# Optimization experiments

Measured on AMD Instinct MI355X. Metric: run time of the kernel, lower is better.

The kernel has to match this reference:

```python
import jax, jax.numpy as jnp
import numpy as np

N_NODES, N_EDGES, HID = 30000, 480000, 128
N_GRAPHS, N_CLASSES = 128, 6
BN_EPS, ADD_SCORE = 1e-5, 0.5


def setup_inputs():
    key = jax.random.key(0)
    ks = jax.random.split(key, 12)
    g = lambda i, shape: jax.random.normal(ks[i], shape, jnp.float32) * 0.05
    return dict(
        x=jax.random.normal(ks[0], (N_NODES, HID), jnp.float32),
        edge_index=jax.random.randint(ks[1], (2, N_EDGES), 0, N_NODES, jnp.int32),
        batch=jnp.sort(jax.random.randint(ks[2], (N_NODES,), 0, N_GRAPHS, jnp.int32)),
        Wl=g(3, (6, HID, HID)), bl=jnp.zeros((6, HID), jnp.float32),
        Wr=g(4, (6, HID, HID)),
        gamma=jnp.ones((6, HID), jnp.float32), beta=jnp.zeros((6, HID), jnp.float32),
        Wlin=g(5, (3, HID, 2 * HID)), blin=jnp.zeros((3, HID), jnp.float32),
        Wp=g(6, (3, 2 * HID)), bp=jnp.zeros((3,), jnp.float32),
        Wf1=g(7, (HID, HID)), bf1=jnp.zeros((HID,), jnp.float32),
        Wf2=g(8, (N_CLASSES, HID)), bf2=jnp.zeros((N_CLASSES,), jnp.float32),
    )


def _sage(x, src, dst, emf, Wl_i, bl_i, Wr_i, N):
    # PyG SAGEConv: lin_l(mean_{j->i} x_j) + lin_r(x_i); emf masks dead edges
    msg = x[src] * emf[:, None]                              # [E,H]
    s = jax.ops.segment_sum(msg, dst, num_segments=N)
    c = jax.ops.segment_sum(emf, dst, num_segments=N)
    mean = s / jnp.maximum(c, 1.0)[:, None]
    return mean @ Wl_i.T + bl_i + x @ Wr_i.T


def _bn(x, g, b, nvf):
    # training-mode BatchNorm over valid (non-merged-away) nodes only
    cnt = jnp.maximum(nvf.sum(), 1.0)
    mu = (x * nvf[:, None]).sum(0) / cnt
    var = (((x - mu) ** 2) * nvf[:, None]).sum(0) / cnt
    return g * (x - mu) * jax.lax.rsqrt(var + BN_EPS) + b


def _edge_pool(x, src, dst, emb, nvb, Wp_i, bp_i, N, E):
    h = x.shape[1]
    # raw edge score = Linear(cat(x[src], x[dst]))
    raw = (x @ Wp_i[:h])[src] + (x @ Wp_i[h:])[dst] + bp_i   # [E]
    neg = jnp.finfo(x.dtype).min
    mx = jax.ops.segment_max(jnp.where(emb, raw, neg), dst, num_segments=N)
    z = jnp.where(emb, jnp.exp(jnp.where(emb, raw - mx[dst], 0.0)), 0.0)
    den = jax.ops.segment_sum(z, dst, num_segments=N)
    score = z / jnp.maximum(den, 1e-16)[dst] + ADD_SCORE     # softmax per dst + 0.5

    # greedy edge matching in descending score order (sequential, int-only carry)
    order = jnp.argsort(-jnp.where(emb, jax.lax.stop_gradient(score), -jnp.inf))

    def step(carry, i):
        matched, cluster, chosen = carry
        s, t = src[i], dst[i]
        ok = emb[i] & (~matched[s]) & (~matched[t]) & (s != t)
        rep, oth = jnp.minimum(s, t), jnp.maximum(s, t)
        matched = matched.at[s].set(matched[s] | ok)
        matched = matched.at[t].set(matched[t] | ok)
        cluster = cluster.at[oth].set(jnp.where(ok, rep, cluster[oth]))
        chosen = chosen.at[rep].set(jnp.where(ok, i, chosen[rep]))
        return (matched, cluster, chosen), None

    init = (~nvb, jnp.arange(N, dtype=jnp.int32), jnp.full((N,), -1, jnp.int32))
    (matched, cluster, chosen), _ = jax.lax.scan(step, init, order)

    # merged node = (x_s + x_t) * score(chosen edge); singleton score = 1
    nscore = jnp.where(chosen >= 0, score[jnp.maximum(chosen, 0)], 1.0)
    new_x = jax.ops.segment_sum(x, cluster, num_segments=N) * nscore[:, None]
    nvb2 = nvb & (cluster == jnp.arange(N, dtype=jnp.int32))
    # remap edges to cluster representatives; coalesce duplicates (self-loops kept, as PyG)
    key = jnp.where(emb, cluster[src] * N + cluster[dst], -1)  # N*N < 2**31
    uk = jnp.unique(key, size=E, fill_value=-1)
    emb2 = uk >= 0
    ukc = jnp.maximum(uk, 0)
    return new_x, ukc // N, ukc % N, emb2, nvb2


def reference(x, edge_index, batch, Wl, bl, Wr, gamma, beta, Wlin, blin, Wp, bp, Wf1, bf1, Wf2, bf2):
    N, E = x.shape[0], edge_index.shape[1]
    src, dst = edge_index[0], edge_index[1]
    emb = jnp.ones((E,), bool)   # edge-valid mask (fixed-shape graph coarsening)
    nvb = jnp.ones((N,), bool)   # node-valid mask
    for blk in range(3):
        emf, nvf = emb.astype(x.dtype), nvb.astype(x.dtype)
        i = 2 * blk
        h = _bn(jax.nn.relu(_sage(x, src, dst, emf, Wl[i], bl[i], Wr[i], N)), gamma[i], beta[i], nvf)
        h2 = _bn(jax.nn.relu(_sage(h, src, dst, emf, Wl[i + 1], bl[i + 1], Wr[i + 1], N)), gamma[i + 1], beta[i + 1], nvf)
        x = jnp.concatenate([h2, h], axis=1) @ Wlin[blk].T + blin[blk]  # dropout = identity (eval)
        x, src, dst, emb, nvb = _edge_pool(x, src, dst, emb, nvb, Wp[blk], bp[blk], N, E)
    nvf = nvb.astype(x.dtype)
    sums = jax.ops.segment_sum(x * nvf[:, None], batch, num_segments=N_GRAPHS)
    cnt = jax.ops.segment_sum(nvf, batch, num_segments=N_GRAPHS)
    pooled = sums / jnp.maximum(cnt, 1.0)[:, None]           # global_mean_pool
    hfc = jax.nn.relu(pooled @ Wf1.T + bf1)
    return jax.nn.log_softmax(hfc @ Wf2.T + bf2, axis=1)
```

## Files before the change

### kernel.cpp

```cpp
#include <hip/hip_runtime.h>
#include <stdint.h>

#define NN 30000
#define NE 480000
#define HID 128
#define NG 128
#define NC 6
#define BN_EPS 1e-5f
#define WPB 938
#define SLOTS 4
#define GPAD 132

typedef unsigned int u32;
typedef unsigned long long u64;

__device__ __forceinline__ u64 ent_key(int4 ent) {
  return ((u64)(u32)ent.y << 32) | (u32)ent.x;
}

__global__ void k_init(const int* __restrict__ ei, int* srcA, int* dstA, int* nvb,
                       int* scal, int* b3, int* i2, float* gbuf) {
  int t = blockIdx.x * 256 + threadIdx.x;
  if (t < NE) { srcA[t] = ei[t]; dstA[t] = ei[NE + t]; }
  if (t < NN) nvb[t] = 1;
  if (t < 2 * NN) { b3[t] = 0; i2[t] = 0; }
  if (t < NG * HID + NG) gbuf[t] = 0.f;
  if (t == 0) { scal[0] = NE; scal[1] = 0; }
}

__global__ void k_csr_count(const int* __restrict__ pE, const int* __restrict__ src,
                            const int* __restrict__ dst, int* __restrict__ cnt,
                            int* __restrict__ icnt, const int* __restrict__ nvb,
                            int* __restrict__ pcnt) {
  int t = blockIdx.x * 256 + threadIdx.x;
  if (t < NN && nvb[t]) atomicAdd(pcnt, 1);
  if (t < *pE) {
    int s = src[t], d = dst[t];
    atomicAdd(&cnt[d], 1);
    if (s != d) { atomicAdd(&icnt[s], 1); atomicAdd(&icnt[d], 1); }
  }
}

__global__ __launch_bounds__(1024) void k_scan2(const int* __restrict__ in0, int* __restrict__ out0,
                                                const int* __restrict__ in1, int* __restrict__ out1) {
  const int* in = blockIdx.x ? in1 : in0;
  int* out = blockIdx.x ? out1 : out0;
  __shared__ int part[1024];
  int t = threadIdx.x;
  int chunk = (NN + 1023) / 1024;
  int b = t * chunk, e = b + chunk;
  if (b > NN) b = NN;
  if (e > NN) e = NN;
  int s = 0;
  for (int i = b; i < e; i++) s += in[i];
  part[t] = s;
  __syncthreads();
  for (int off = 1; off < 1024; off <<= 1) {
    int v = (t >= off) ? part[t - off] : 0;
    __syncthreads();
    part[t] += v;
    __syncthreads();
  }
  int excl = (t == 0) ? 0 : part[t - 1];
  for (int i = b; i < e; i++) { out[i] = excl; excl += in[i]; }
  if (t == 0) out[NN] = part[1023];
}

__global__ void k_csr_scatter(const int* __restrict__ pE, const int* __restrict__ src,
                              const int* __restrict__ dst, const int* __restrict__ coff,
                              int* __restrict__ cursor, int* __restrict__ eids,
                              int* __restrict__ gsrc) {
  int e = blockIdx.x * 256 + threadIdx.x;
  if (e >= *pE) return;
  int d = dst[e];
  int pos = coff[d] + atomicAdd(&cursor[d], 1);
  eids[pos] = e;
  gsrc[pos] = src[e];
}

__global__ __launch_bounds__(256) void k_sage_gather(
    const int* __restrict__ coff, const int* __restrict__ gsrc,
    const float* __restrict__ x, float* __restrict__ mean,
    double* __restrict__ bnsum) {
  if (blockIdx.x == 0 && threadIdx.x < 2 * HID) bnsum[threadIdx.x] = 0.0;
  int grp = threadIdx.x >> 5;
  int lane = threadIdx.x & 31;
  int n = blockIdx.x * 8 + grp;
  if (n >= NN) return;
  int b = coff[n], e2 = coff[n + 1];
  float4 acc = make_float4(0.f, 0.f, 0.f, 0.f);
  int i = b;
  for (; i + 1 < e2; i += 2) {
    int s0 = gsrc[i], s1 = gsrc[i + 1];
    float4 v0 = *(const float4*)(x + (size_t)s0 * HID + lane * 4);
    float4 v1 = *(const float4*)(x + (size_t)s1 * HID + lane * 4);
    acc.x += v0.x; acc.y += v0.y; acc.z += v0.z; acc.w += v0.w;
    acc.x += v1.x; acc.y += v1.y; acc.z += v1.z; acc.w += v1.w;
  }
  if (i < e2) {
    int s0 = gsrc[i];
    float4 v0 = *(const float4*)(x + (size_t)s0 * HID + lane * 4);
    acc.x += v0.x; acc.y += v0.y; acc.z += v0.z; acc.w += v0.w;
  }
  float inv = 1.0f / fmaxf((float)(e2 - b), 1.0f);
  acc.x *= inv; acc.y *= inv; acc.z *= inv; acc.w *= inv;
  *(float4*)(mean + (size_t)n * HID + lane * 4) = acc;
}

__global__ __launch_bounds__(256) void gemm_dual2(
    const float* __restrict__ A1, const float* __restrict__ W1,
    const float* __restrict__ A2, const float* __restrict__ W2,
    const float* __restrict__ bias, float* __restrict__ out,
    int M, int ldw, int relu, const int* __restrict__ nvb,
    double* __restrict__ bnsum, int dostats) {
  __shared__ float Ast[16][GPAD];
  __shared__ float Ws[16][GPAD];
  int tid = threadIdx.x;
  int rg = tid >> 4, cg = tid & 15;
  int r0 = rg * 8, c0 = cg * 8;
  int row0 = blockIdx.x * 128;
  float acc[8][8];
#pragma unroll
  for (int a = 0; a < 8; a++)
#pragma unroll
    for (int bq = 0; bq < 8; bq++) acc[a][bq] = 0.f;

  for (int srcI = 0; srcI < 2; srcI++) {
    const float* A = srcI ? A2 : A1;
    const float* W = srcI ? W2 : W1;
    for (int kc = 0; kc < 128; kc += 16) {
#pragma unroll
      for (int i = 0; i < 2; i++) {
        int k = tid + i * 256;
        int r = k >> 2, c4 = (k & 3) << 2;
        int gr = row0 + r;
        float4 v = make_float4(0.f, 0.f, 0.f, 0.f);
        if (gr < M) v = *(const float4*)(A + (size_t)gr * 128 + kc + c4);
        Ast[c4 + 0][r] = v.x; Ast[c4 + 1][r] = v.y;
        Ast[c4 + 2][r] = v.z; Ast[c4 + 3][r] = v.w;
        float4 w = *(const float4*)(W + (size_t)r * ldw + kc + c4);
        Ws[c4 + 0][r] = w.x; Ws[c4 + 1][r] = w.y;
        Ws[c4 + 2][r] = w.z; Ws[c4 + 3][r] = w.w;
      }
      __syncthreads();
#pragma unroll
      for (int kk = 0; kk < 16; kk++) {
        float4 a0 = *(const float4*)(&Ast[kk][r0]);
        float4 a1 = *(const float4*)(&Ast[kk][r0 + 4]);
        float4 b0 = *(const float4*)(&Ws[kk][c0]);
        float4 b1 = *(const float4*)(&Ws[kk][c0 + 4]);
        float av[8] = {a0.x, a0.y, a0.z, a0.w, a1.x, a1.y, a1.z, a1.w};
        float bv[8] = {b0.x, b0.y, b0.z, b0.w, b1.x, b1.y, b1.z, b1.w};
#pragma unroll
        for (int rr = 0; rr < 8; rr++)
#pragma unroll
          for (int cc = 0; cc < 8; cc++) acc[rr][cc] += av[rr] * bv[cc];
      }
      __syncthreads();
    }
  }

  float sCol[8], qCol[8];
#pragma unroll
  for (int cc = 0; cc < 8; cc++) { sCol[cc] = 0.f; qCol[cc] = 0.f; }
#pragma unroll
  for (int rr = 0; rr < 8; rr++) {
    int gr = row0 + r0 + rr;
    if (gr >= M) continue;
    int valid = dostats ? nvb[gr] : 0;
    float vv[8];
#pragma unroll
    for (int cc = 0; cc < 8; cc++) {
      float v = acc[rr][cc] + bias[c0 + cc];
      if (relu) v = fmaxf(v, 0.f);
      vv[cc] = v;
      if (valid) { sCol[cc] += v; qCol[cc] += v * v; }
    }
    *(float4*)(out + (size_t)gr * 128 + c0) = make_float4(vv[0], vv[1], vv[2], vv[3]);
    *(float4*)(out + (size_t)gr * 128 + c0 + 4) = make_float4(vv[4], vv[5], vv[6], vv[7]);
  }
  if (dostats) {
#pragma unroll
    for (int cc = 0; cc < 8; cc++) { Ast[rg][c0 + cc] = sCol[cc]; Ws[rg][c0 + cc] = qCol[cc]; }
    __syncthreads();
    if (tid < HID) {
      float s = 0.f, q = 0.f;
#pragma unroll
      for (int g = 0; g < 16; g++) { s += Ast[g][tid]; q += Ws[g][tid]; }
      atomicAdd(&bnsum[tid], (double)s);
      atomicAdd(&bnsum[HID + tid], (double)q);
    }
  }
}

__global__ void k_bn_apply(float* __restrict__ x, const double* __restrict__ sums,
                           const int* __restrict__ cnt, const float* __restrict__ gamma,
                           const float* __restrict__ beta) {
  int t = blockIdx.x * 256 + threadIdx.x;
  if (t >= NN * HID) return;
  int k = t & 127;
  double c = (double)((*cnt > 1) ? *cnt : 1);
  double mu = sums[k] / c;
  double var = sums[HID + k] / c - mu * mu;
  if (var < 0.0) var = 0.0;
  float inv = (float)(1.0 / sqrt(var + (double)BN_EPS));
  x[t] = gamma[k] * (x[t] - (float)mu) * inv + beta[k];
}

__global__ void k_node_proj(const float* __restrict__ x, const float* __restrict__ Wp,
                            float* __restrict__ px1, float* __restrict__ px2) {
  int n = blockIdx.x * 256 + threadIdx.x;
  if (n >= NN) return;
  const float* xr = x + (size_t)n * HID;
  float s1 = 0.f, s2 = 0.f;
#pragma unroll 8
  for (int k = 0; k < HID; k += 4) {
    float4 v = *(const float4*)(xr + k);
    float4 w1 = *(const float4*)(Wp + k);
    float4 w2 = *(const float4*)(Wp + HID + k);
    s1 += v.x * w1.x + v.y * w1.y + v.z * w1.z + v.w * w1.w;
    s2 += v.x * w2.x + v.y * w2.y + v.z * w2.z + v.w * w2.w;
  }
  px1[n] = s1; px2[n] = s2;
}

__global__ void k_edge_softmax_seed(
    const int* __restrict__ coff, const int* __restrict__ eids,
    const int* __restrict__ gsrc, const float* __restrict__ px1,
    const float* __restrict__ px2, const float* __restrict__ bp,
    float* __restrict__ score, u64* __restrict__ ekey, u64* __restrict__ S) {
  int n = blockIdx.x * 256 + threadIdx.x;
  if (n >= NN) return;
  S[n] = 0ull;
  int b = coff[n], e2 = coff[n + 1];
  if (b == e2) return;
  float p2 = px2[n] + *bp;
  float mx = -3.4e38f;
  for (int i = b; i < e2; i++) {
    float r = px1[gsrc[i]] + p2;
    mx = fmaxf(mx, r);
  }
  double den = 0.0;
  for (int i = b; i < e2; i++) {
    int eid = eids[i];
    float z = expf(px1[gsrc[i]] + p2 - mx);
    score[eid] = z;
    den += (double)z;
  }
  if (den < 1e-16) den = 1e-16;
  double invd = 1.0 / den;
  for (int i = b; i < e2; i++) {
    int eid = eids[i];
    float sc = (float)((double)score[eid] * invd) + 0.5f;
    score[eid] = sc;
    ekey[eid] = ((u64)__float_as_uint(sc) << 32) | (u64)(0xFFFFFFFFu - (u32)eid);
  }
}

__global__ void k_inc_scatter(const int* __restrict__ pE, const int* __restrict__ src,
                              const int* __restrict__ dst, const u64* __restrict__ ekey,
                              const int* __restrict__ ioff, int* __restrict__ icur,
                              int4* __restrict__ ielist) {
  int e = blockIdx.x * 256 + threadIdx.x;
  if (e >= *pE) return;
  int s = src[e], d = dst[e];
  if (s == d) return;
  u64 k = ekey[e];
  int4 ent;
  ent.x = (int)(u32)(k & 0xFFFFFFFFull);
  ent.y = (int)(u32)(k >> 32);
  ent.w = 0;
  ent.z = d;
  ielist[ioff[s] + atomicAdd(&icur[s], 1)] = ent;
  ent.z = s;
  ielist[ioff[d] + atomicAdd(&icur[d], 1)] = ent;
}

__global__ __launch_bounds__(256) void k_suitor(
    const int* __restrict__ ioff, const int4* __restrict__ ielist,
    const int* __restrict__ src, const int* __restrict__ dst,
    u64* __restrict__ S) {
  int wid = threadIdx.x >> 6;
  int lane = threadIdx.x & 63;
  int n = blockIdx.x * 4 + wid;
  if (n >= NN) return;
  int cur = n;
  while (cur >= 0) {
    int b = ioff[cur], e2 = ioff[cur + 1];
    int deg = e2 - b;
    if (deg == 0) break;
    if (deg <= 64 * SLOTS) {
      u64 key[SLOTS]; int pv[SLOTS];
#pragma unroll
      for (int s = 0; s < SLOTS; s++) {
        key[s] = 0; pv[s] = 0;
        int i = b + s * 64 + lane;
        if (i < e2) {
          int4 ent = ielist[i];
          key[s] = ent_key(ent);
          pv[s] = ent.z;
        }
      }
      long long res;
      for (;;) {
        u64 localBest = 0;
#pragma unroll
        for (int s = 0; s < SLOTS; s++) {
          if (!key[s]) continue;
          u64 sv = __hip_atomic_load(&S[pv[s]], __ATOMIC_RELAXED, __HIP_MEMORY_SCOPE_AGENT);
          if (sv >= key[s]) key[s] = 0;
          else if (key[s] > localBest) localBest = key[s];
        }
        u64 bestKey = localBest;
#pragma unroll
        for (int o = 32; o > 0; o >>= 1) {
          u64 other = __shfl_xor(bestKey, o, 64);
          if (other > bestKey) bestKey = other;
        }
        if (bestKey == 0) { res = -1; break; }
        int ms = -1;
#pragma unroll
        for (int s = 0; s < SLOTS; s++)
          if (ms < 0 && key[s] == bestKey) ms = s;
        u64 ball = __ballot(ms >= 0);
        int owner = (int)(__ffsll((long long)ball) - 1);
        long long r0 = -3;
        if (lane == owner) {
          int bv = pv[ms];
          u64 old = atomicMax(&S[bv], bestKey);
          if (old >= bestKey) { key[ms] = 0; r0 = -2; }
          else if (old == 0) r0 = -1;
          else {
            int eo = (int)(0xFFFFFFFFu - (u32)(old & 0xFFFFFFFFull));
            int so = src[eo], do_ = dst[eo];
            r0 = (so == bv) ? do_ : so;
          }
        }
        res = __shfl(r0, owner, 64);
        if (res != -2) break;
      }
      if (res < 0) break;
      cur = (int)res;
    } else {
      u64 bestKey = 0;
      for (int i = b + lane; i < e2; i += 64) {
        int4 ent = ielist[i];
        u64 k = ent_key(ent);
        if (k <= bestKey) continue;
        u64 sv = __hip_atomic_load(&S[ent.z], __ATOMIC_RELAXED, __HIP_MEMORY_SCOPE_AGENT);
        if (k > sv) bestKey = k;
      }
#pragma unroll
      for (int o = 32; o > 0; o >>= 1) {
        u64 other = __shfl_xor(bestKey, o, 64);
        if (other > bestKey) bestKey = other;
      }
      long long r0 = -1;
      if (bestKey != 0 && lane == 0) {
        int e = (int)(0xFFFFFFFFu - (u32)(bestKey & 0xFFFFFFFFull));
        int es = src[e], ed = dst[e];
        int bv = (es == cur) ? ed : es;
        u64 old = atomicMax(&S[bv], bestKey);
        if (old >= bestKey) r0 = cur;
        else if (old != 0) {
          int eo = (int)(0xFFFFFFFFu - (u32)(old & 0xFFFFFFFFull));
          int so = src[eo], do_ = dst[eo];
          r0 = (so == bv) ? do_ : so;
        }
      }
      long long res = (bestKey != 0) ? __shfl(r0, 0, 64) : -1;
      cur = (int)res;
    }
  }
}

__global__ __launch_bounds__(256) void k_new_x(
    const u64* __restrict__ S, const int* __restrict__ src, const int* __restrict__ dst,
    const float* __restrict__ score, const float* __restrict__ x,
    float* __restrict__ out, int* __restrict__ cluster,
    int* __restrict__ nvb, int* __restrict__ b3zero) {
  int gt = blockIdx.x * 256 + threadIdx.x;
  if (gt < 2 * NN) b3zero[gt] = 0;
  int grp = threadIdx.x >> 5;
  int lane = threadIdx.x & 31;
  int n = blockIdx.x * 8 + grp;
  if (n >= NN) return;
  u64 k = S[n];
  int partner = -1;
  int rep = n;
  bool isOth = false;
  float sc = 1.f;
  if (k) {
    int e = (int)(0xFFFFFFFFu - (u32)(k & 0xFFFFFFFFull));
    int s = src[e], d = dst[e];
    int other = (s == n) ? d : s;
    if (S[other] == k) {
      if (n > other) { isOth = true; rep = other; }
      else { partner = other; sc = score[e]; }
    }
  }
  float4 v = make_float4(0.f, 0.f, 0.f, 0.f);
  if (!isOth) {
    v = *(const float4*)(x + (size_t)n * HID + lane * 4);
    if (partner >= 0) {
      float4 w = *(const float4*)(x + (size_t)partner * HID + lane * 4);
      v.x = (v.x + w.x) * sc; v.y = (v.y + w.y) * sc;
      v.z = (v.z + w.z) * sc; v.w = (v.w + w.w) * sc;
    }
  }
  *(float4*)(out + (size_t)n * HID + lane * 4) = v;
  if (lane == 0) {
    cluster[n] = rep;
    nvb[n] = (nvb[n] && !isOth) ? 1 : 0;
  }
}

__global__ void k_bucket_count(const int* __restrict__ pE, const int* __restrict__ src,
                               const int* __restrict__ cluster, int* __restrict__ bcount) {
  int e = blockIdx.x * 256 + threadIdx.x;
  if (e >= *pE) return;
  atomicAdd(&bcount[cluster[src[e]]], 1);
}

__global__ __launch_bounds__(1024) void k_scan(const int* __restrict__ in, int* __restrict__ out,
                                               int n, int* totalDst) {
  __shared__ int part[1024];
  int t = threadIdx.x;
  int chunk = (n + 1023) / 1024;
  int b = t * chunk, e = b + chunk;
  if (b > n) b = n;
  if (e > n) e = n;
  int s = 0;
  for (int i = b; i < e; i++) s += in[i];
  part[t] = s;
  __syncthreads();
  for (int off = 1; off < 1024; off <<= 1) {
    int v = (t >= off) ? part[t - off] : 0;
    __syncthreads();
    part[t] += v;
    __syncthreads();
  }
  int excl = (t == 0) ? 0 : part[t - 1];
  int total = part[1023];
  for (int i = b; i < e; i++) { out[i] = excl; excl += in[i]; }
  if (t == 0) {
    out[n] = total;
    if (totalDst) *totalDst = total;
  }
}

__global__ void k_bucket_scatter(const int* __restrict__ pE, const int* __restrict__ src,
                                 const int* __restrict__ dst, const int* __restrict__ cluster,
                                 const int* __restrict__ boffs, int* __restrict__ bcursor,
                                 int* __restrict__ bucket) {
  int e = blockIdx.x * 256 + threadIdx.x;
  if (e >= *pE) return;
  int cs = cluster[src[e]], cd = cluster[dst[e]];
  int pos = boffs[cs] + atomicAdd(&bcursor[cs], 1);
  bucket[pos] = cd;
}

__global__ __launch_bounds__(256) void k_dedup_bitmap(
    const int* __restrict__ boffs, int* __restrict__ bucket,
    int* __restrict__ ucount) {
  __shared__ u32 bm[4][960];
  int wid = threadIdx.x >> 6;
  int lane = threadIdx.x & 63;
  int n = blockIdx.x * 4 + wid;
  int b = boffs[n], e = boffs[n + 1];
  for (int w = lane; w < 960; w += 64) bm[wid][w] = 0;
  __syncthreads();
  for (int i = b + lane; i < e; i += 64)
    atomicOr(&bm[wid][bucket[i] >> 5], 1u << (bucket[i] & 31));
  __syncthreads();
  int w0 = lane * 15;
  int w1 = w0 + 15; if (w1 > WPB) w1 = WPB;
  int cnt = 0;
  for (int w = w0; w < w1; w++) cnt += __popc(bm[wid][w]);
  int inc = cnt;
  for (int o = 1; o < 64; o <<= 1) { int v = __shfl_up(inc, o); if (lane >= o) inc += v; }
  int excl = inc - cnt;
  int total = __shfl(inc, 63);
  int pos = b + excl;
  for (int w = w0; w < w1; w++) {
    u32 v = bm[wid][w];
    while (v) { int bit = __ffs(v) - 1; bucket[pos++] = (w << 5) | bit; v &= v - 1; }
  }
  if (lane == 0) ucount[n] = total;
}

__global__ void k_emit(const int* __restrict__ boffs, const int* __restrict__ bucket,
                       const int* __restrict__ bucount, const int* __restrict__ bnoffs,
                       int* __restrict__ srcO, int* __restrict__ dstO,
                       int* __restrict__ b3zero, int* __restrict__ i2zero,
                       int* __restrict__ pcnt) {
  int t = blockIdx.x * 256 + threadIdx.x;
  int stride = gridDim.x * 256;
  for (int z = t; z < 2 * NN; z += stride) { b3zero[z] = 0; i2zero[z] = 0; }
  if (t == 0) *pcnt = 0;
  if (t >= NN) return;
  int u = bucount[t], b = boffs[t], o = bnoffs[t];
  for (int i = 0; i < u; i++) { srcO[o + i] = t; dstO[o + i] = bucket[b + i]; }
}

__global__ void k_graph_pool(const int* __restrict__ nvb, const int* __restrict__ batch,
                             const float* __restrict__ x, float* __restrict__ gsum,
                             float* __restrict__ gcnt) {
  int t = blockIdx.x * 256 + threadIdx.x;
  int n = t >> 2;
  if (n >= NN) return;
  if (!nvb[n]) return;
  int sub = t & 3;
  int g = batch[n];
  const float* xr = x + (size_t)n * HID + sub * 32;
  float* o = gsum + (size_t)g * HID + sub * 32;
#pragma unroll
  for (int i = 0; i < 8; i++) {
    float4 v = *(const float4*)(xr + i * 4);
    atomicAdd(o + i * 4 + 0, v.x); atomicAdd(o + i * 4 + 1, v.y);
    atomicAdd(o + i * 4 + 2, v.z); atomicAdd(o + i * 4 + 3, v.w);
  }
  if (sub == 0) atomicAdd(&gcnt[g], 1.0f);
}

__global__ __launch_bounds__(128) void k_head1(const float* __restrict__ gsum,
                                               const float* __restrict__ gcnt,
                                               const float* __restrict__ Wf1,
                                               const float* __restrict__ bf1,
                                               float* __restrict__ hfc) {
  int g = blockIdx.x;
  int j = threadIdx.x;
  __shared__ float p[HID];
  float c = fmaxf(gcnt[g], 1.f);
  p[j] = gsum[g * HID + j] / c;
  __syncthreads();
  float s = bf1[j];
  const float* w = Wf1 + (size_t)j * HID;
  for (int k = 0; k < HID; k++) s += p[k] * w[k];
  hfc[g * HID + j] = fmaxf(s, 0.f);
}

__global__ void k_head2(const float* __restrict__ hfc, const float* __restrict__ Wf2,
                        const float* __restrict__ bf2, float* __restrict__ out) {
  int g = blockIdx.x;
  int t = threadIdx.x;
  __shared__ float lg[NC];
  if (t < NC) {
    float s = bf2[t];
    const float* w = Wf2 + (size_t)t * HID;
    const float* h = hfc + (size_t)g * HID;
    for (int k = 0; k < HID; k++) s += h[k] * w[k];
    lg[t] = s;
  }
  __syncthreads();
  if (t == 0) {
    float m = lg[0];
    for (int c = 1; c < NC; c++) m = fmaxf(m, lg[c]);
    float se = 0.f;
    for (int c = 0; c < NC; c++) se += expf(lg[c] - m);
    float lse = m + logf(se);
    for (int c = 0; c < NC; c++) out[g * NC + c] = lg[c] - lse;
  }
}

extern "C" void kernel_launch(void* const* d_in, const int* in_sizes, int n_in,
                              void* d_out, int out_size, void* d_ws, size_t ws_size,
                              hipStream_t stream) {
  const float* x0 = (const float*)d_in[0];
  const int* ei = (const int*)d_in[1];
  const int* batch = (const int*)d_in[2];
  const float* Wl = (const float*)d_in[3];
  const float* bl = (const float*)d_in[4];
  const float* Wr = (const float*)d_in[5];
  const float* gamma = (const float*)d_in[6];
  const float* beta = (const float*)d_in[7];
  const float* Wlin = (const float*)d_in[8];
  const float* blin = (const float*)d_in[9];
  const float* Wp = (const float*)d_in[10];
  const float* bp = (const float*)d_in[11];
  const float* Wf1 = (const float*)d_in[12];
  const float* bf1 = (const float*)d_in[13];
  const float* Wf2 = (const float*)d_in[14];
  const float* bf2 = (const float*)d_in[15];
  float* out = (float*)d_out;

  const int NH = NN * HID;
  size_t off = 0;
  char* base = (char*)d_ws;
  auto carve = [&](size_t bytes) -> char* {
    char* p = base + off;
    off += (bytes + 255) & ~(size_t)255;
    return p;
  };
  float* xa = (float*)carve((size_t)NH * 4);
  float* xb = (float*)carve((size_t)NH * 4);
  float* xc = (float*)carve((size_t)NH * 4);
  float* xd = (float*)carve((size_t)NH * 4);
  int* srcA = (int*)carve((size_t)NE * 4);
  int* dstA = (int*)carve((size_t)NE * 4);
  int* srcB = (int*)carve((size_t)NE * 4);
  int* dstB = (int*)carve((size_t)NE * 4);
  float* escore = (float*)carve((size_t)NE * 4);
  int* ebucket = (int*)carve((size_t)NE * 4);
  int* eids = (int*)carve((size_t)NE * 4);
  int* gsrc = (int*)carve((size_t)NE * 4);
  u64* ekey = (u64*)carve((size_t)NE * 8);
  u64* S = (u64*)carve((size_t)NN * 8);
  float* npx1 = (float*)carve((size_t)NN * 4);
  float* npx2 = (float*)carve((size_t)NN * 4);
  int* ncluster = (int*)carve((size_t)NN * 4);
  int* nvb = (int*)carve((size_t)NN * 4);
  int* b3 = (int*)carve((size_t)3 * NN * 4);
  int* bcount = b3;
  int* bcursor = b3 + NN;
  int* bucount = b3 + 2 * NN;
  int* i2 = (int*)carve((size_t)2 * NN * 4);
  int* icnt = i2;
  int* icursor = i2 + NN;
  int* boffs = (int*)carve((size_t)(NN + 1) * 4);
  int* bnoffs = (int*)carve((size_t)(NN + 1) * 4);
  int* csroff = (int*)carve((size_t)(NN + 1) * 4);
  int* ioff = (int*)carve((size_t)(NN + 1) * 4);
  double* bnsum = (double*)carve((size_t)2 * HID * 8);
  float* gbuf = (float*)carve((size_t)(NG * HID + NG) * 4);
  float* gsum = gbuf;
  float* gcnt = gbuf + NG * HID;
  float* ghfc = (float*)carve((size_t)NG * HID * 4);
  int* scal = (int*)carve(64 * 4);
  (void)ws_size; (void)n_in; (void)in_sizes; (void)out_size;

  int4* ielist = (int4*)xc;

  int* pE = scal;
  int* pcnt = scal + 1;

  k_init<<<1875, 256, 0, stream>>>(ei, srcA, dstA, nvb, scal, b3, i2, gbuf);

  int* srcC = srcA; int* dstC = dstA; int* srcN = srcB; int* dstN = dstB;
  float* xcur = xa;
  float* xtmp = xd;

  auto sage = [&](const float* xin, float* xout, int L) {
    k_sage_gather<<<3750, 256, 0, stream>>>(csroff, gsrc, xin, xtmp, bnsum);
    gemm_dual2<<<235, 256, 0, stream>>>(xtmp, Wl + (size_t)L * HID * HID, xin,
                                        Wr + (size_t)L * HID * HID, bl + (size_t)L * HID,
                                        xout, NN, HID, 1, nvb, bnsum, 1);
    k_bn_apply<<<15000, 256, 0, stream>>>(xout, bnsum, pcnt, gamma + (size_t)L * HID,
                                          beta + (size_t)L * HID);
  };

  for (int b = 0; b < 3; b++) {
    const float* xin = (b == 0) ? x0 : (const float*)xcur;

    k_csr_count<<<1875, 256, 0, stream>>>(pE, srcC, dstC, bcount, icnt, nvb, pcnt);
    k_scan2<<<2, 1024, 0, stream>>>(bcount, csroff, icnt, ioff);
    k_csr_scatter<<<1875, 256, 0, stream>>>(pE, srcC, dstC, csroff, bcursor, eids, gsrc);

    sage(xin, xb, 2 * b);
    sage(xb, xc, 2 * b + 1);
    gemm_dual2<<<235, 256, 0, stream>>>(xc, Wlin + (size_t)b * HID * 2 * HID, xb,
                                        Wlin + (size_t)b * HID * 2 * HID + HID,
                                        blin + (size_t)b * HID, xcur, NN, 2 * HID, 0,
                                        nvb, bnsum, 0);

    k_node_proj<<<118, 256, 0, stream>>>(xcur, Wp + (size_t)b * 2 * HID, npx1, npx2);
    k_edge_softmax_seed<<<118, 256, 0, stream>>>(csroff, eids, gsrc, npx1, npx2, bp + b,
                                                 escore, ekey, S);
    k_inc_scatter<<<1875, 256, 0, stream>>>(pE, srcC, dstC, ekey, ioff, icursor, ielist);
    k_suitor<<<7500, 256, 0, stream>>>(ioff, ielist, srcC, dstC, S);
    k_new_x<<<3750, 256, 0, stream>>>(S, srcC, dstC, escore, xcur, xtmp,
                                      ncluster, nvb, b3);

    if (b < 2) {
      k_bucket_count<<<1875, 256, 0, stream>>>(pE, srcC, ncluster, bcount);
      k_scan<<<1, 1024, 0, stream>>>(bcount, boffs, NN, (int*)nullptr);
      k_bucket_scatter<<<1875, 256, 0, stream>>>(pE, srcC, dstC, ncluster, boffs, bcursor,
                                                 ebucket);
      k_dedup_bitmap<<<7500, 256, 0, stream>>>(boffs, ebucket, bucount);
      k_scan<<<1, 1024, 0, stream>>>(bucount, bnoffs, NN, pE);
      k_emit<<<235, 256, 0, stream>>>(boffs, ebucket, bucount, bnoffs, srcN, dstN,
                                      b3, i2, pcnt);
      { int* t = srcC; srcC = srcN; srcN = t; t = dstC; dstC = dstN; dstN = t; }
    }
    { float* t = xcur; xcur = xtmp; xtmp = t; }
  }

  k_graph_pool<<<469, 256, 0, stream>>>(nvb, batch, xcur, gsum, gcnt);
  k_head1<<<NG, 128, 0, stream>>>(gsum, gcnt, Wf1, bf1, ghfc);
  k_head2<<<NG, 32, 0, stream>>>(ghfc, Wf2, bf2, out);
}
```

Baseline: 2.544 ms.

## Fold BatchNorm into next GEMM load, fuse node projection, restructure suitor kernel

```diff
diff --git a/kernel.cpp b/kernel.cpp
--- a/kernel.cpp
+++ b/kernel.cpp
@@ -19,12 +19,14 @@
 }
 
 __global__ void k_init(const int* __restrict__ ei, int* srcA, int* dstA, int* nvb,
-                       int* scal, int* b3, int* i2, float* gbuf) {
+                       int* scal, int* b3, int* i2, float* gbuf,
+                       double* __restrict__ bnsum) {
   int t = blockIdx.x * 256 + threadIdx.x;
   if (t < NE) { srcA[t] = ei[t]; dstA[t] = ei[NE + t]; }
   if (t < NN) nvb[t] = 1;
   if (t < 2 * NN) { b3[t] = 0; i2[t] = 0; }
   if (t < NG * HID + NG) gbuf[t] = 0.f;
+  if (t < 2 * HID) bnsum[t] = 0.0;
   if (t == 0) { scal[0] = NE; scal[1] = 0; }
 }
 
@@ -80,9 +82,7 @@
 
 __global__ __launch_bounds__(256) void k_sage_gather(
     const int* __restrict__ coff, const int* __restrict__ gsrc,
-    const float* __restrict__ x, float* __restrict__ mean,
-    double* __restrict__ bnsum) {
-  if (blockIdx.x == 0 && threadIdx.x < 2 * HID) bnsum[threadIdx.x] = 0.0;
+    const float* __restrict__ x, float* __restrict__ mean) {
   int grp = threadIdx.x >> 5;
   int lane = threadIdx.x & 31;
   int n = blockIdx.x * 8 + grp;
@@ -112,7 +112,10 @@
     const float* __restrict__ A2, const float* __restrict__ W2,
     const float* __restrict__ bias, float* __restrict__ out,
     int M, int ldw, int relu, const int* __restrict__ nvb,
-    double* __restrict__ bnsum, int dostats) {
+    double* __restrict__ bnsum, int dostats,
+    const float* __restrict__ a1f, const float* __restrict__ c1f,
+    const float* __restrict__ a2f, const float* __restrict__ c2f,
+    const float* __restrict__ Wp, float* __restrict__ px1, float* __restrict__ px2) {
   __shared__ float Ast[16][GPAD];
   __shared__ float Ws[16][GPAD];
   int tid = threadIdx.x;
@@ -128,6 +131,8 @@
   for (int srcI = 0; srcI < 2; srcI++) {
     const float* A = srcI ? A2 : A1;
     const float* W = srcI ? W2 : W1;
+    const float* fa = srcI ? a2f : a1f;
+    const float* fc = srcI ? c2f : c1f;
     for (int kc = 0; kc < 128; kc += 16) {
 #pragma unroll
       for (int i = 0; i < 2; i++) {
@@ -136,6 +141,12 @@
         int gr = row0 + r;
         float4 v = make_float4(0.f, 0.f, 0.f, 0.f);
         if (gr < M) v = *(const float4*)(A + (size_t)gr * 128 + kc + c4);
+        if (fa) {
+          float4 av = *(const float4*)(fa + kc + c4);
+          float4 cv = *(const float4*)(fc + kc + c4);
+          v.x = v.x * av.x + cv.x; v.y = v.y * av.y + cv.y;
+          v.z = v.z * av.z + cv.z; v.w = v.w * av.w + cv.w;
+        }
         Ast[c4 + 0][r] = v.x; Ast[c4 + 1][r] = v.y;
         Ast[c4 + 2][r] = v.z; Ast[c4 + 3][r] = v.w;
         float4 w = *(const float4*)(W + (size_t)r * ldw + kc + c4);
@@ -160,24 +171,45 @@
     }
   }
 
+  float wp1[8], wp2[8];
+  if (Wp) {
+#pragma unroll
+    for (int cc = 0; cc < 8; cc++) { wp1[cc] = Wp[c0 + cc]; wp2[cc] = Wp[HID + c0 + cc]; }
+  }
+  float* part1 = (float*)Ast;
+  float* part2 = (float*)Ws;
   float sCol[8], qCol[8];
 #pragma unroll
   for (int cc = 0; cc < 8; cc++) { sCol[cc] = 0.f; qCol[cc] = 0.f; }
 #pragma unroll
   for (int rr = 0; rr < 8; rr++) {
     int gr = row0 + r0 + rr;
-    if (gr >= M) continue;
-    int valid = dostats ? nvb[gr] : 0;
-    float vv[8];
-#pragma unroll
-    for (int cc = 0; cc < 8; cc++) {
-      float v = acc[rr][cc] + bias[c0 + cc];
-      if (relu) v = fmaxf(v, 0.f);
-      vv[cc] = v;
-      if (valid) { sCol[cc] += v; qCol[cc] += v * v; }
+    float p1 = 0.f, p2 = 0.f;
+    if (gr < M) {
+      int valid = dostats ? nvb[gr] : 0;
+      float vv[8];
+#pragma unroll
+      for (int cc = 0; cc < 8; cc++) {
+        float v = acc[rr][cc] + bias[c0 + cc];
+        if (relu) v = fmaxf(v, 0.f);
+        vv[cc] = v;
+        if (valid) { sCol[cc] += v; qCol[cc] += v * v; }
+        if (Wp) { p1 += v * wp1[cc]; p2 += v * wp2[cc]; }
+      }
+      *(float4*)(out + (size_t)gr * 128 + c0) = make_float4(vv[0], vv[1], vv[2], vv[3]);
+      *(float4*)(out + (size_t)gr * 128 + c0 + 4) = make_float4(vv[4], vv[5], vv[6], vv[7]);
     }
-    *(float4*)(out + (size_t)gr * 128 + c0) = make_float4(vv[0], vv[1], vv[2], vv[3]);
-    *(float4*)(out + (size_t)gr * 128 + c0 + 4) = make_float4(vv[4], vv[5], vv[6], vv[7]);
+    if (Wp) { part1[(r0 + rr) * 16 + cg] = p1; part2[(r0 + rr) * 16 + cg] = p2; }
+  }
+  if (Wp) {
+    __syncthreads();
+    if (tid < HID && row0 + tid < M) {
+      float s1 = 0.f, s2 = 0.f;
+#pragma unroll
+      for (int g = 0; g < 16; g++) { s1 += part1[tid * 16 + g]; s2 += part2[tid * 16 + g]; }
+      px1[row0 + tid] = s1;
+      px2[row0 + tid] = s2;
+    }
   }
   if (dostats) {
 #pragma unroll
@@ -193,35 +225,20 @@
   }
 }
 
-__global__ void k_bn_apply(float* __restrict__ x, const double* __restrict__ sums,
-                           const int* __restrict__ cnt, const float* __restrict__ gamma,
-                           const float* __restrict__ beta) {
-  int t = blockIdx.x * 256 + threadIdx.x;
-  if (t >= NN * HID) return;
-  int k = t & 127;
+__global__ void k_bnfold(double* __restrict__ bnsum, const int* __restrict__ cnt,
+                         const float* __restrict__ gamma, const float* __restrict__ beta,
+                         float* __restrict__ affa, float* __restrict__ affc) {
+  int k = threadIdx.x;
   double c = (double)((*cnt > 1) ? *cnt : 1);
-  double mu = sums[k] / c;
-  double var = sums[HID + k] / c - mu * mu;
+  double mu = bnsum[k] / c;
+  double var = bnsum[HID + k] / c - mu * mu;
   if (var < 0.0) var = 0.0;
-  float inv = (float)(1.0 / sqrt(var + (double)BN_EPS));
-  x[t] = gamma[k] * (x[t] - (float)mu) * inv + beta[k];
-}
-
-__global__ void k_node_proj(const float* __restrict__ x, const float* __restrict__ Wp,
-                            float* __restrict__ px1, float* __restrict__ px2) {
-  int n = blockIdx.x * 256 + threadIdx.x;
-  if (n >= NN) return;
-  const float* xr = x + (size_t)n * HID;
-  float s1 = 0.f, s2 = 0.f;
-#pragma unroll 8
-  for (int k = 0; k < HID; k += 4) {
-    float4 v = *(const float4*)(xr + k);
-    float4 w1 = *(const float4*)(Wp + k);
-    float4 w2 = *(const float4*)(Wp + HID + k);
-    s1 += v.x * w1.x + v.y * w1.y + v.z * w1.z + v.w * w1.w;
-    s2 += v.x * w2.x + v.y * w2.y + v.z * w2.z + v.w * w2.w;
-  }
-  px1[n] = s1; px2[n] = s2;
+  double inv = 1.0 / sqrt(var + (double)BN_EPS);
+  double a = (double)gamma[k] * inv;
+  affa[k] = (float)a;
+  affc[k] = (float)((double)beta[k] - mu * a);
+  bnsum[k] = 0.0;
+  bnsum[HID + k] = 0.0;
 }
 
 __global__ void k_edge_softmax_seed(
@@ -276,15 +293,12 @@
   ielist[ioff[d] + atomicAdd(&icur[d], 1)] = ent;
 }
 
-__global__ __launch_bounds__(256) void k_suitor(
+__global__ __launch_bounds__(64) void k_suitor(
     const int* __restrict__ ioff, const int4* __restrict__ ielist,
     const int* __restrict__ src, const int* __restrict__ dst,
     u64* __restrict__ S) {
-  int wid = threadIdx.x >> 6;
-  int lane = threadIdx.x & 63;
-  int n = blockIdx.x * 4 + wid;
-  if (n >= NN) return;
-  int cur = n;
+  int lane = threadIdx.x;
+  int cur = blockIdx.x;
   while (cur >= 0) {
     int b = ioff[cur], e2 = ioff[cur + 1];
     int deg = e2 - b;
@@ -301,17 +315,18 @@
           pv[s] = ent.z;
         }
       }
+#pragma unroll
+      for (int s = 0; s < SLOTS; s++) {
+        if (!key[s]) continue;
+        u64 sv = __hip_atomic_load(&S[pv[s]], __ATOMIC_RELAXED, __HIP_MEMORY_SCOPE_AGENT);
+        if (sv >= key[s]) key[s] = 0;
+      }
       long long res;
       for (;;) {
-        u64 localBest = 0;
-#pragma unroll
-        for (int s = 0; s < SLOTS; s++) {
-          if (!key[s]) continue;
-          u64 sv = __hip_atomic_load(&S[pv[s]], __ATOMIC_RELAXED, __HIP_MEMORY_SCOPE_AGENT);
-          if (sv >= key[s]) key[s] = 0;
-          else if (key[s] > localBest) localBest = key[s];
-        }
-        u64 bestKey = localBest;
+        u64 bestKey = 0;
+#pragma unroll
+        for (int s = 0; s < SLOTS; s++)
+          if (key[s] > bestKey) bestKey = key[s];
 #pragma unroll
         for (int o = 32; o > 0; o >>= 1) {
           u64 other = __shfl_xor(bestKey, o, 64);
@@ -622,6 +637,10 @@
   int* csroff = (int*)carve((size_t)(NN + 1) * 4);
   int* ioff = (int*)carve((size_t)(NN + 1) * 4);
   double* bnsum = (double*)carve((size_t)2 * HID * 8);
+  float* affa1 = (float*)carve((size_t)HID * 4);
+  float* affc1 = (float*)carve((size_t)HID * 4);
+  float* affa2 = (float*)carve((size_t)HID * 4);
+  float* affc2 = (float*)carve((size_t)HID * 4);
   float* gbuf = (float*)carve((size_t)(NG * HID + NG) * 4);
   float* gsum = gbuf;
   float* gcnt = gbuf + NG * HID;
@@ -634,19 +653,18 @@
   int* pE = scal;
   int* pcnt = scal + 1;
 
-  k_init<<<1875, 256, 0, stream>>>(ei, srcA, dstA, nvb, scal, b3, i2, gbuf);
+  k_init<<<1875, 256, 0, stream>>>(ei, srcA, dstA, nvb, scal, b3, i2, gbuf, bnsum);
 
   int* srcC = srcA; int* dstC = dstA; int* srcN = srcB; int* dstN = dstB;
   float* xcur = xa;
   float* xtmp = xd;
 
-  auto sage = [&](const float* xin, float* xout, int L) {
-    k_sage_gather<<<3750, 256, 0, stream>>>(csroff, gsrc, xin, xtmp, bnsum);
+  auto sage = [&](const float* xin, float* xout, int L, const float* fa, const float* fc) {
+    k_sage_gather<<<3750, 256, 0, stream>>>(csroff, gsrc, xin, xtmp);
     gemm_dual2<<<235, 256, 0, stream>>>(xtmp, Wl + (size_t)L * HID * HID, xin,
                                         Wr + (size_t)L * HID * HID, bl + (size_t)L * HID,
-                                        xout, NN, HID, 1, nvb, bnsum, 1);
-    k_bn_apply<<<15000, 256, 0, stream>>>(xout, bnsum, pcnt, gamma + (size_t)L * HID,
-                                          beta + (size_t)L * HID);
+                                        xout, NN, HID, 1, nvb, bnsum, 1,
+                                        fa, fc, fa, fc, nullptr, nullptr, nullptr);
   };
 
   for (int b = 0; b < 3; b++) {
@@ -656,18 +674,22 @@
     k_scan2<<<2, 1024, 0, stream>>>(bcount, csroff, icnt, ioff);
     k_csr_scatter<<<1875, 256, 0, stream>>>(pE, srcC, dstC, csroff, bcursor, eids, gsrc);
 
-    sage(xin, xb, 2 * b);
-    sage(xb, xc, 2 * b + 1);
+    sage(xin, xb, 2 * b, nullptr, nullptr);
+    k_bnfold<<<1, 128, 0, stream>>>(bnsum, pcnt, gamma + (size_t)(2 * b) * HID,
+                                    beta + (size_t)(2 * b) * HID, affa1, affc1);
+    sage(xb, xc, 2 * b + 1, affa1, affc1);
+    k_bnfold<<<1, 128, 0, stream>>>(bnsum, pcnt, gamma + (size_t)(2 * b + 1) * HID,
+                                    beta + (size_t)(2 * b + 1) * HID, affa2, affc2);
     gemm_dual2<<<235, 256, 0, stream>>>(xc, Wlin + (size_t)b * HID * 2 * HID, xb,
                                         Wlin + (size_t)b * HID * 2 * HID + HID,
                                         blin + (size_t)b * HID, xcur, NN, 2 * HID, 0,
-                                        nvb, bnsum, 0);
-
-    k_node_proj<<<118, 256, 0, stream>>>(xcur, Wp + (size_t)b * 2 * HID, npx1, npx2);
+                                        nvb, bnsum, 0, affa2, affc2, affa1, affc1,
+                                        Wp + (size_t)b * 2 * HID, npx1, npx2);
+
     k_edge_softmax_seed<<<118, 256, 0, stream>>>(csroff, eids, gsrc, npx1, npx2, bp + b,
                                                  escore, ekey, S);
     k_inc_scatter<<<1875, 256, 0, stream>>>(pE, srcC, dstC, ekey, ioff, icursor, ielist);
-    k_suitor<<<7500, 256, 0, stream>>>(ioff, ielist, srcC, dstC, S);
+    k_suitor<<<30000, 64, 0, stream>>>(ioff, ielist, srcC, dstC, S);
     k_new_x<<<3750, 256, 0, stream>>>(S, srcC, dstC, escore, xcur, xtmp,
                                       ncluster, nvb, b3);
 
```

Result: no change. 2.526 ms (-0.7%).
